# Performance work log

Measured on AMD Instinct MI355X. Metric: run time of the kernel, lower is better.

The kernel has to match this reference:

```python
import jax, jax.numpy as jnp
import numpy as np

DIM, HEADS, SEG, DIL = 1024, 16, 64, 2
B, L = 4, 4096
HEAD_DIM = DIM // HEADS
SCALE = HEAD_DIM ** -0.5


def _hilbert_map(seq_len: int) -> np.ndarray:
    # exact port of generate_hilbert_curve / hilbert_index
    size = int(np.ceil(np.sqrt(seq_len)))
    if size * size != seq_len:
        size = 2 ** int(np.ceil(np.log2(size)))

    def hidx(x, y, n):
        d = 0
        s = n // 2
        while s > 0:
            rx = 1 if (x & s) > 0 else 0
            ry = 1 if (y & s) > 0 else 0
            d += s * s * ((3 * rx) ^ ry)
            if ry == 0:
                if rx == 1:
                    x = n - 1 - x
                    y = n - 1 - y
                x, y = y, x
            s //= 2
        return d

    m = np.zeros(size * size, dtype=np.int32)
    for y in range(size):
        for x in range(size):
            m[y * size + x] = hidx(x, y, size)
    return m[:seq_len]


def setup_inputs() -> dict:
    key = jax.random.key(0)
    k1, k2, k3 = jax.random.split(key, 3)
    x = jax.random.normal(k1, (B, L, DIM), dtype=jnp.float32)
    w_qkv = jax.random.normal(k2, (DIM, 3 * DIM), dtype=jnp.float32) * 0.02
    w_proj = jax.random.normal(k3, (DIM, DIM), dtype=jnp.float32) * 0.02
    hilbert_map = jnp.asarray(_hilbert_map(L))
    return {"x": x, "w_qkv": w_qkv, "w_proj": w_proj, "hilbert_map": hilbert_map}


def reference(x, w_qkv, w_proj, hilbert_map):
    Bq, Lq, _ = x.shape
    n_seg = Lq // SEG
    # qkv projection -> [3, B, H, L, D]
    qkv = (x @ w_qkv).reshape(Bq, Lq, 3, HEADS, HEAD_DIM).transpose(2, 0, 3, 1, 4)
    q, k, v = qkv[0], qkv[1], qkv[2]
    # Hilbert reorder along sequence
    q = q[:, :, hilbert_map, :]
    k = k[:, :, hilbert_map, :]
    v = v[:, :, hilbert_map, :]
    # segmented dilated attention: [B,H,S,seg,D]
    qs = q.reshape(Bq, HEADS, n_seg, SEG, HEAD_DIM)
    ks = k.reshape(Bq, HEADS, n_seg, SEG, HEAD_DIM)[:, :, :, ::DIL, :]
    vs = v.reshape(Bq, HEADS, n_seg, SEG, HEAD_DIM)[:, :, :, ::DIL, :]
    scores = jnp.einsum('bhsqd,bhskd->bhsqk', qs, ks) * SCALE
    attn = jax.nn.softmax(scores, axis=-1)
    out = jnp.einsum('bhsqk,bhskd->bhsqd', attn, vs).reshape(Bq, HEADS, Lq, HEAD_DIM)
    # inverse Hilbert reorder
    inv = jnp.argsort(hilbert_map)
    out = out[:, :, inv, :]
    out = out.transpose(0, 2, 1, 3).reshape(Bq, Lq, DIM)
    return out @ w_proj
```

## Files before the change

### kernel.cpp

```cpp
#include <hip/hip_runtime.h>

#define L_SEQ 4096

typedef unsigned short u16;
typedef unsigned int u32;
typedef __bf16 bf16_t;
typedef bf16_t bf16x8 __attribute__((ext_vector_type(8)));
typedef float f32x4 __attribute__((ext_vector_type(4)));
typedef unsigned short u16x8 __attribute__((ext_vector_type(8)));

__device__ __forceinline__ u16 f2b(float f) {
  unsigned u = __float_as_uint(f);
  u += 0x7fffu + ((u >> 16) & 1u);
  return (u16)(u >> 16);
}
__device__ __forceinline__ float b2f(u16 b) {
  return __uint_as_float(((unsigned)b) << 16);
}

#define FENCE asm volatile("" ::: "memory")
#define BARRIER __builtin_amdgcn_s_barrier()
#define WAIT_LGKM0 asm volatile("s_waitcnt lgkmcnt(0)" ::: "memory")
#define WAIT_VM4 asm volatile("s_waitcnt vmcnt(4)" ::: "memory")
#define SB0 __builtin_amdgcn_sched_barrier(0)
#define AS1 __attribute__((address_space(1)))
#define AS3 __attribute__((address_space(3)))

__global__ __launch_bounds__(256) void k_prep(const float* __restrict__ x,
                                              u16* __restrict__ xb,
                                              const float* __restrict__ wq,
                                              u16* __restrict__ wqT,
                                              const float* __restrict__ wp,
                                              u16* __restrict__ wpT,
                                              const int* __restrict__ hmap,
                                              u16* __restrict__ xg) {
  const int bid = blockIdx.x;
  const int t = threadIdx.x;
  if (bid < 4096) {
    const int i = (bid * 256 + t) * 16;
    f32x4 v0 = *reinterpret_cast<const f32x4*>(x + i);
    f32x4 v1 = *reinterpret_cast<const f32x4*>(x + i + 4);
    f32x4 v2 = *reinterpret_cast<const f32x4*>(x + i + 8);
    f32x4 v3 = *reinterpret_cast<const f32x4*>(x + i + 12);
    u16x8 o0, o1;
#pragma unroll
    for (int j = 0; j < 4; ++j) {
      o0[j] = f2b(v0[j]); o0[4 + j] = f2b(v1[j]);
      o1[j] = f2b(v2[j]); o1[4 + j] = f2b(v3[j]);
    }
    *reinterpret_cast<u16x8*>(xb + i) = o0;
    *reinterpret_cast<u16x8*>(xb + i + 8) = o1;
    return;
  }
  if (bid >= 8192) {
    const int g = bid - 8192;
    const int gi = g * 8 + (t >> 5);
    const int lane32 = t & 31;
    const int b = gi >> 11, i = gi & 2047;
    const int s = i >> 5, j = i & 31;
    const int token = hmap[s * 64 + 2 * j];
    const float* src = x + ((size_t)(b * 4096 + token)) * 1024 + lane32 * 32;
    u16* dst = xg + (size_t)gi * 1024 + lane32 * 32;
#pragma unroll
    for (int c = 0; c < 4; ++c) {
      f32x4 v0 = *(const f32x4*)(src + c * 8);
      f32x4 v1 = *(const f32x4*)(src + c * 8 + 4);
      u16x8 o;
#pragma unroll
      for (int q = 0; q < 4; ++q) { o[q] = f2b(v0[q]); o[4 + q] = f2b(v1[q]); }
      *(u16x8*)(dst + c * 8) = o;
    }
    return;
  }
  const float* in; u16* out; int R, C, bx, by;
  if (bid < 7168) {
    const int b2 = bid - 4096;
    in = wq; out = wqT; R = 1024; C = 3072;
    bx = (b2 % 96) * 32; by = (b2 / 96) * 32;
  } else {
    const int b2 = bid - 7168;
    in = wp; out = wpT; R = 1024; C = 1024;
    bx = (b2 % 32) * 32; by = (b2 / 32) * 32;
  }
  __shared__ float tile[32][33];
  const int tx = t & 31, ty = t >> 5;
#pragma unroll
  for (int i = 0; i < 32; i += 8)
    tile[ty + i][tx] = in[(size_t)(by + ty + i) * C + (bx + tx)];
  __syncthreads();
#pragma unroll
  for (int i = 0; i < 32; i += 8)
    out[(size_t)(bx + ty + i) * R + (by + tx)] = f2b(tile[tx][ty + i]);
}

template <bool OUT_BF16>
__device__ __forceinline__ void gemm_body(char* lds, const u16* __restrict__ A,
                                          const u16* __restrict__ Bt,
                                          void* __restrict__ Cv,
                                          int N, int K, int ntiles, int gx, int bid) {
  const int tid = threadIdx.x;
  const int wid = tid >> 6, lane = tid & 63;
  const int wm = wid >> 2, wn = wid & 3;
  const int lr = lane & 15, lq = lane >> 4;
  const int xr = (lr & 7) << 4;
  const int koff0 = (lq * 16) ^ xr;
  const int koff1 = (64 | (lq * 16)) ^ xr;

  const int cpx = 32 * ntiles;
  auto tilecoord = [&](int ff, int& mm, int& nn) {
    int swz = (ff & 7) * cpx + (ff >> 3);
    mm = (swz / gx) * 256; nn = (swz % gx) * 256;
  };

  const int rowT = tid >> 3;
  const int colT = (((tid * 16) & 127) ^ ((rowT & 7) << 4)) >> 1;
  const size_t r64K = (size_t)64 * K;
  const size_t r128K = (size_t)128 * K;

  int m0, n0;
  tilecoord(bid, m0, n0);
  const u16* pAc = A + (size_t)(m0 + rowT) * K + colT;
  const u16* pBc = Bt + (size_t)(n0 + rowT) * K + colT;

  f32x4 acc[8][4];
  bf16x8 a[4][2];
  bf16x8 bb[2][2][2];

  auto STG = [&](const u16* bp, int region, size_t hoff, int k0) {
    const u16* s0 = bp + hoff + k0;
    __builtin_amdgcn_global_load_lds((const AS1 void*)s0,
                                     (AS3 void*)(lds + region + wid * 1024), 16, 0, 0);
    __builtin_amdgcn_global_load_lds((const AS1 void*)(s0 + r64K),
                                     (AS3 void*)(lds + region + 8192 + wid * 1024), 16, 0, 0);
  };
  auto rdA = [&](int dbuf, int mh) {
#pragma unroll
    for (int mi = 0; mi < 4; ++mi) {
      const int base = dbuf * 65536 + wm * 16384 + (mh * 64 + mi * 16 + lr) * 128;
      a[mi][0] = *(const bf16x8*)(lds + base + koff0);
      a[mi][1] = *(const bf16x8*)(lds + base + koff1);
    }
  };
  auto rdB = [&](int dbuf, int nh, int bset) {
#pragma unroll
    for (int ni = 0; ni < 2; ++ni) {
      const int base = dbuf * 65536 + 32768 + (wn >> 1) * 16384 +
                       ((wn & 1) * 64 + nh * 32 + ni * 16 + lr) * 128;
      bb[bset][ni][0] = *(const bf16x8*)(lds + base + koff0);
      bb[bset][ni][1] = *(const bf16x8*)(lds + base + koff1);
    }
  };
  auto mfma16 = [&](int mh, int nh, int bset) {
    __builtin_amdgcn_s_setprio(1);
#pragma unroll
    for (int kk = 0; kk < 2; ++kk)
#pragma unroll
      for (int ni = 0; ni < 2; ++ni)
#pragma unroll
        for (int mi = 0; mi < 4; ++mi)
          acc[mh * 4 + mi][nh * 2 + ni] = __builtin_amdgcn_mfma_f32_16x16x32_bf16(
              a[mi][kk], bb[bset][ni][kk], acc[mh * 4 + mi][nh * 2 + ni], 0, 0, 0);
    __builtin_amdgcn_s_setprio(0);
  };

  STG(pAc, 0,             0,     0);
  STG(pBc, 32768,         0,     0);
  STG(pBc, 49152,         r128K, 0);
  STG(pAc, 16384,         r128K, 0);
  STG(pBc, 65536 + 32768, 0,     64);
  STG(pBc, 65536 + 49152, r128K, 64);
  WAIT_VM4; FENCE; BARRIER;

  const int NT = K >> 6;
  const int NI = NT >> 1;

  for (int tt = 0; tt < ntiles; ++tt) {
    const bool hasn = (tt + 1 < ntiles);
    int m0n = m0, n0n = n0;
    if (hasn) tilecoord(bid + (tt + 1) * 256, m0n, n0n);
    const u16* pAn = hasn ? (A + (size_t)(m0n + rowT) * K + colT) : pAc;
    const u16* pBn = hasn ? (Bt + (size_t)(n0n + rowT) * K + colT) : pBc;

    {
      f32x4 z = {0.f, 0.f, 0.f, 0.f};
#pragma unroll
      for (int i = 0; i < 8; ++i)
#pragma unroll
        for (int j = 0; j < 4; ++j) acc[i][j] = z;
    }

    for (int it = 0; it < NI; ++it) {
      const int kP1 = (2 * it + 1) * 64;
      const bool last = (it == NI - 1);
      const int kA = last ? 0 : (2 * it + 2) * 64;
      const int kB = last ? 64 : (2 * it + 3) * 64;
      const u16* sA = last ? pAn : pAc;
      const u16* sB = last ? pBn : pBc;

      rdA(0, 0); rdB(0, 0, 0);
      STG(pAc, 65536, 0, kP1);
      FENCE; BARRIER; WAIT_LGKM0; SB0;
      mfma16(0, 0, 0);
      FENCE; BARRIER;
      rdB(0, 1, 1);
      STG(pAc, 65536 + 16384, r128K, kP1);
      FENCE; BARRIER; WAIT_LGKM0; SB0;
      mfma16(0, 1, 1);
      FENCE; BARRIER;
      rdA(0, 1);
      STG(sB, 32768, 0, kA);
      STG(sB, 49152, r128K, kA);
      FENCE; BARRIER; WAIT_LGKM0; SB0;
      mfma16(1, 1, 1);
      mfma16(1, 0, 0);
      WAIT_VM4; FENCE; BARRIER;
      rdA(1, 0); rdB(1, 0, 0);
      STG(sA, 0, 0, kA);
      FENCE; BARRIER; WAIT_LGKM0; SB0;
      mfma16(0, 0, 0);
      FENCE; BARRIER;
      rdB(1, 1, 1);
      STG(sA, 16384, r128K, kA);
      FENCE; BARRIER; WAIT_LGKM0; SB0;
      mfma16(0, 1, 1);
      FENCE; BARRIER;
      rdA(1, 1);
      STG(sB, 65536 + 32768, 0, kB);
      STG(sB, 65536 + 49152, r128K, kB);
      FENCE; BARRIER; WAIT_LGKM0; SB0;
      mfma16(1, 1, 1);
      mfma16(1, 0, 0);
      WAIT_VM4; FENCE; BARRIER;
    }

#pragma unroll
    for (int mi = 0; mi < 8; ++mi)
#pragma unroll
      for (int ni = 0; ni < 4; ++ni) {
        const int r0 = m0 + wm * 128 + (mi >> 2) * 64 + (mi & 3) * 16 + lq * 4;
        const int c = n0 + wn * 64 + (ni >> 1) * 32 + (ni & 1) * 16 + lr;
#pragma unroll
        for (int r = 0; r < 4; ++r) {
          const float v = acc[mi][ni][r];
          if (OUT_BF16)
            ((u16*)Cv)[(size_t)(r0 + r) * N + c] = f2b(v);
          else
            ((float*)Cv)[(size_t)(r0 + r) * N + c] = v;
        }
      }

    m0 = m0n; n0 = n0n; pAc = pAn; pBc = pBn;
  }
}

__global__ __launch_bounds__(512, 2) void k_gemm_qkv(const u16* __restrict__ xb,
                                                     const u16* __restrict__ xg,
                                                     const u16* __restrict__ wT,
                                                     u16* __restrict__ qb,
                                                     u16* __restrict__ kvb) {
  __shared__ __align__(16) char lds[131072];
  const bool kv = (blockIdx.x >= 256);
  gemm_body<true>(lds,
                  kv ? xg : xb,
                  kv ? (wT + 1024 * 1024) : wT,
                  kv ? (void*)kvb : (void*)qb,
                  kv ? 2048 : 1024, 1024, 1, kv ? 8 : 4,
                  blockIdx.x & 255);
}

__global__ __launch_bounds__(512, 2) void k_gemm_proj(const u16* __restrict__ A,
                                                      const u16* __restrict__ Bt,
                                                      float* __restrict__ C) {
  __shared__ __align__(16) char lds[131072];
  gemm_body<false>(lds, A, Bt, C, 1024, 1024, 1, 4, blockIdx.x);
}

__global__ __launch_bounds__(256) void k_attn2(const u16* __restrict__ qb,
                                               const u16* __restrict__ kvb,
                                               const int* __restrict__ hmap,
                                               u16* __restrict__ att) {
  __shared__ u16 VT[64 * 40];
  __shared__ u16 Pl[4][16 * 40];

  const int blk = blockIdx.x;
  const int b = blk >> 10, h = (blk >> 6) & 15, s = blk & 63;
  const int t = threadIdx.x, w = t >> 6, lane = t & 63;
  const int lr = lane & 15, lq = lane >> 4;
  const int* hm = hmap + s * 64;
  const size_t bb4 = (size_t)b * L_SEQ;
  const size_t kvrow0 = (size_t)(b * 2048 + s * 32);

  {
    const int kj = t >> 3, d0 = (t & 7) * 8;
    const u16* p = kvb + (kvrow0 + kj) * 2048 + 1024 + h * 64 + d0;
    u16x8 v = *(const u16x8*)p;
#pragma unroll
    for (int j = 0; j < 8; ++j) {
      const int d = d0 + j;
      const int chunk = (kj >> 3) ^ ((d >> 3) & 3);
      VT[d * 40 + chunk * 8 + (kj & 7)] = v[j];
    }
  }

  const u16* qp = qb + (bb4 + hm[16 * w + lr]) * 1024 + h * 64 + lq * 8;
  bf16x8 aq0 = *(const bf16x8*)(qp);
  bf16x8 aq1 = *(const bf16x8*)(qp + 32);
  bf16x8 bk[2][2];
#pragma unroll
  for (int nk = 0; nk < 2; ++nk) {
    const u16* kp = kvb + (kvrow0 + nk * 16 + lr) * 2048 + h * 64 + lq * 8;
    bk[nk][0] = *(const bf16x8*)(kp);
    bk[nk][1] = *(const bf16x8*)(kp + 32);
  }

  f32x4 z4 = {0.f, 0.f, 0.f, 0.f};
  f32x4 s0 = __builtin_amdgcn_mfma_f32_16x16x32_bf16(aq0, bk[0][0], z4, 0, 0, 0);
  s0 = __builtin_amdgcn_mfma_f32_16x16x32_bf16(aq1, bk[0][1], s0, 0, 0, 0);
  f32x4 s1 = __builtin_amdgcn_mfma_f32_16x16x32_bf16(aq0, bk[1][0], z4, 0, 0, 0);
  s1 = __builtin_amdgcn_mfma_f32_16x16x32_bf16(aq1, bk[1][1], s1, 0, 0, 0);

  float inv[4];
  u16* Pw = Pl[w];
#pragma unroll
  for (int r = 0; r < 4; ++r) {
    float a0 = s0[r] * 0.125f, a1 = s1[r] * 0.125f;
    float m = fmaxf(a0, a1);
    m = fmaxf(m, __shfl_xor(m, 1));
    m = fmaxf(m, __shfl_xor(m, 2));
    m = fmaxf(m, __shfl_xor(m, 4));
    m = fmaxf(m, __shfl_xor(m, 8));
    float e0 = __expf(a0 - m), e1 = __expf(a1 - m);
    float sum = e0 + e1;
    sum += __shfl_xor(sum, 1);
    sum += __shfl_xor(sum, 2);
    sum += __shfl_xor(sum, 4);
    sum += __shfl_xor(sum, 8);
    inv[r] = 1.f / sum;
    Pw[(lq * 4 + r) * 40 + lr] = f2b(e0);
    Pw[(lq * 4 + r) * 40 + 16 + lr] = f2b(e1);
  }

  __syncthreads();

  bf16x8 ap = *(const bf16x8*)(Pw + lr * 40 + lq * 8);
  f32x4 o[4];
#pragma unroll
  for (int nd = 0; nd < 4; ++nd) {
    const int row = nd * 16 + lr;
    const int chunk = lq ^ ((row >> 3) & 3);
    bf16x8 bv = *(const bf16x8*)(VT + row * 40 + chunk * 8);
    o[nd] = __builtin_amdgcn_mfma_f32_16x16x32_bf16(ap, bv, z4, 0, 0, 0);
  }

#pragma unroll
  for (int r = 0; r < 4; ++r) {
    u16* dst = att + (bb4 + hm[16 * w + lq * 4 + r]) * 1024 + h * 64 + lr;
#pragma unroll
    for (int nd = 0; nd < 4; ++nd)
      dst[nd * 16] = f2b(o[nd][r] * inv[r]);
  }
}

extern "C" void kernel_launch(void* const* d_in, const int* in_sizes, int n_in,
                              void* d_out, int out_size, void* d_ws, size_t ws_size,
                              hipStream_t stream) {
  const float* x = (const float*)d_in[0];
  const float* w_qkv = (const float*)d_in[1];
  const float* w_proj = (const float*)d_in[2];
  const int* hmap = (const int*)d_in[3];
  float* out = (float*)d_out;

  char* ws = (char*)d_ws;
  u16* qb    = (u16*)(ws);
  u16* kvb   = (u16*)(ws + 33554432ull);
  u16* xb    = (u16*)(ws + 67108864ull);
  u16* xg    = (u16*)(ws + 100663296ull);
  u16* wqkvT = (u16*)(ws + 117440512ull);
  u16* wpT   = (u16*)(ws + 123731968ull);
  u16* att = xb;

  k_prep<<<9216, 256, 0, stream>>>(x, xb, w_qkv, wqkvT, w_proj, wpT, hmap, xg);
  k_gemm_qkv<<<512, 512, 0, stream>>>(xb, xg, wqkvT, qb, kvb);
  k_attn2<<<4096, 256, 0, stream>>>(qb, kvb, hmap, att);
  k_gemm_proj<<<256, 512, 0, stream>>>(att, wpT, out);
}
```

Measured before the change: 166.5 us.

## Fuse Hilbert gather of K/V rows into QKV GEMM A-loads, drop xg buffer

Removes the prep-kernel pass that gathered and converted Hilbert-selected x rows into a separate xg buffer. The KV half of the QKV GEMM now computes per-row source pointers through hmap and loads scattered rows of xb directly into LDS. The multi-tile loop in gemm_body is also removed and each block handles exactly one tile. This saves a global read and write of about 16 MB plus 1024 prep blocks, at the cost of non-contiguous A-row loads in the GEMM.

```diff
diff --git a/kernel.cpp b/kernel.cpp
--- a/kernel.cpp
+++ b/kernel.cpp
@@ -31,9 +31,7 @@
                                               const float* __restrict__ wq,
                                               u16* __restrict__ wqT,
                                               const float* __restrict__ wp,
-                                              u16* __restrict__ wpT,
-                                              const int* __restrict__ hmap,
-                                              u16* __restrict__ xg) {
+                                              u16* __restrict__ wpT) {
   const int bid = blockIdx.x;
   const int t = threadIdx.x;
   if (bid < 4096) {
@@ -52,26 +50,6 @@
     *reinterpret_cast<u16x8*>(xb + i + 8) = o1;
     return;
   }
-  if (bid >= 8192) {
-    const int g = bid - 8192;
-    const int gi = g * 8 + (t >> 5);
-    const int lane32 = t & 31;
-    const int b = gi >> 11, i = gi & 2047;
-    const int s = i >> 5, j = i & 31;
-    const int token = hmap[s * 64 + 2 * j];
-    const float* src = x + ((size_t)(b * 4096 + token)) * 1024 + lane32 * 32;
-    u16* dst = xg + (size_t)gi * 1024 + lane32 * 32;
-#pragma unroll
-    for (int c = 0; c < 4; ++c) {
-      f32x4 v0 = *(const f32x4*)(src + c * 8);
-      f32x4 v1 = *(const f32x4*)(src + c * 8 + 4);
-      u16x8 o;
-#pragma unroll
-      for (int q = 0; q < 4; ++q) { o[q] = f2b(v0[q]); o[4 + q] = f2b(v1[q]); }
-      *(u16x8*)(dst + c * 8) = o;
-    }
-    return;
-  }
   const float* in; u16* out; int R, C, bx, by;
   if (bid < 7168) {
     const int b2 = bid - 4096;
@@ -93,11 +71,12 @@
     out[(size_t)(bx + ty + i) * R + (by + tx)] = f2b(tile[tx][ty + i]);
 }
 
-template <bool OUT_BF16>
+template <bool OUT_BF16, bool AMAP>
 __device__ __forceinline__ void gemm_body(char* lds, const u16* __restrict__ A,
                                           const u16* __restrict__ Bt,
+                                          const int* __restrict__ hmap,
                                           void* __restrict__ Cv,
-                                          int N, int K, int ntiles, int gx, int bid) {
+                                          int N, int K, int gx, int bid) {
   const int tid = threadIdx.x;
   const int wid = tid >> 6, lane = tid & 63;
   const int wm = wid >> 2, wn = wid & 3;
@@ -106,32 +85,46 @@
   const int koff0 = (lq * 16) ^ xr;
   const int koff1 = (64 | (lq * 16)) ^ xr;
 
-  const int cpx = 32 * ntiles;
-  auto tilecoord = [&](int ff, int& mm, int& nn) {
-    int swz = (ff & 7) * cpx + (ff >> 3);
-    mm = (swz / gx) * 256; nn = (swz % gx) * 256;
-  };
+  const int swz = (bid & 7) * 32 + (bid >> 3);
+  const int m0 = (swz / gx) * 256, n0 = (swz % gx) * 256;
 
   const int rowT = tid >> 3;
   const int colT = (((tid * 16) & 127) ^ ((rowT & 7) << 4)) >> 1;
   const size_t r64K = (size_t)64 * K;
   const size_t r128K = (size_t)128 * K;
 
-  int m0, n0;
-  tilecoord(bid, m0, n0);
-  const u16* pAc = A + (size_t)(m0 + rowT) * K + colT;
+  const u16 *pA0, *pA1, *pA2, *pA3;
+  if constexpr (AMAP) {
+    auto maprow = [&](int gi) -> const u16* {
+      const int token = hmap[((gi & 2047) >> 5) * 64 + 2 * (gi & 31)];
+      return A + ((size_t)((gi >> 11) * 4096 + token)) * (size_t)K + colT;
+    };
+    pA0 = maprow(m0 + rowT);
+    pA1 = maprow(m0 + 64 + rowT);
+    pA2 = maprow(m0 + 128 + rowT);
+    pA3 = maprow(m0 + 192 + rowT);
+  } else {
+    pA0 = A + (size_t)(m0 + rowT) * K + colT;
+    pA1 = pA0 + r64K; pA2 = pA0 + r128K; pA3 = pA2 + r64K;
+  }
   const u16* pBc = Bt + (size_t)(n0 + rowT) * K + colT;
 
   f32x4 acc[8][4];
   bf16x8 a[4][2];
   bf16x8 bb[2][2][2];
 
-  auto STG = [&](const u16* bp, int region, size_t hoff, int k0) {
-    const u16* s0 = bp + hoff + k0;
+  auto LDS1 = [&](const u16* s0, int region) {
     __builtin_amdgcn_global_load_lds((const AS1 void*)s0,
                                      (AS3 void*)(lds + region + wid * 1024), 16, 0, 0);
-    __builtin_amdgcn_global_load_lds((const AS1 void*)(s0 + r64K),
-                                     (AS3 void*)(lds + region + 8192 + wid * 1024), 16, 0, 0);
+  };
+  auto STG_A0 = [&](int region, int k0) {
+    LDS1(pA0 + k0, region); LDS1(pA1 + k0, region + 8192);
+  };
+  auto STG_A1 = [&](int region, int k0) {
+    LDS1(pA2 + k0, region); LDS1(pA3 + k0, region + 8192);
+  };
+  auto STG_B = [&](int region, size_t hoff, int k0) {
+    LDS1(pBc + hoff + k0, region); LDS1(pBc + hoff + r64K + k0, region + 8192);
   };
   auto rdA = [&](int dbuf, int mh) {
 #pragma unroll
@@ -163,116 +156,101 @@
     __builtin_amdgcn_s_setprio(0);
   };
 
-  STG(pAc, 0,             0,     0);
-  STG(pBc, 32768,         0,     0);
-  STG(pBc, 49152,         r128K, 0);
-  STG(pAc, 16384,         r128K, 0);
-  STG(pBc, 65536 + 32768, 0,     64);
-  STG(pBc, 65536 + 49152, r128K, 64);
+  {
+    f32x4 z = {0.f, 0.f, 0.f, 0.f};
+#pragma unroll
+    for (int i = 0; i < 8; ++i)
+#pragma unroll
+      for (int j = 0; j < 4; ++j) acc[i][j] = z;
+  }
+
+  STG_A0(0, 0);
+  STG_B(32768, 0, 0);
+  STG_B(49152, r128K, 0);
+  STG_A1(16384, 0);
+  STG_B(65536 + 32768, 0, 64);
+  STG_B(65536 + 49152, r128K, 64);
   WAIT_VM4; FENCE; BARRIER;
 
-  const int NT = K >> 6;
-  const int NI = NT >> 1;
-
-  for (int tt = 0; tt < ntiles; ++tt) {
-    const bool hasn = (tt + 1 < ntiles);
-    int m0n = m0, n0n = n0;
-    if (hasn) tilecoord(bid + (tt + 1) * 256, m0n, n0n);
-    const u16* pAn = hasn ? (A + (size_t)(m0n + rowT) * K + colT) : pAc;
-    const u16* pBn = hasn ? (Bt + (size_t)(n0n + rowT) * K + colT) : pBc;
-
-    {
-      f32x4 z = {0.f, 0.f, 0.f, 0.f};
-#pragma unroll
-      for (int i = 0; i < 8; ++i)
-#pragma unroll
-        for (int j = 0; j < 4; ++j) acc[i][j] = z;
-    }
-
-    for (int it = 0; it < NI; ++it) {
-      const int kP1 = (2 * it + 1) * 64;
-      const bool last = (it == NI - 1);
-      const int kA = last ? 0 : (2 * it + 2) * 64;
-      const int kB = last ? 64 : (2 * it + 3) * 64;
-      const u16* sA = last ? pAn : pAc;
-      const u16* sB = last ? pBn : pBc;
-
-      rdA(0, 0); rdB(0, 0, 0);
-      STG(pAc, 65536, 0, kP1);
-      FENCE; BARRIER; WAIT_LGKM0; SB0;
-      mfma16(0, 0, 0);
-      FENCE; BARRIER;
-      rdB(0, 1, 1);
-      STG(pAc, 65536 + 16384, r128K, kP1);
-      FENCE; BARRIER; WAIT_LGKM0; SB0;
-      mfma16(0, 1, 1);
-      FENCE; BARRIER;
-      rdA(0, 1);
-      STG(sB, 32768, 0, kA);
-      STG(sB, 49152, r128K, kA);
-      FENCE; BARRIER; WAIT_LGKM0; SB0;
-      mfma16(1, 1, 1);
-      mfma16(1, 0, 0);
-      WAIT_VM4; FENCE; BARRIER;
-      rdA(1, 0); rdB(1, 0, 0);
-      STG(sA, 0, 0, kA);
-      FENCE; BARRIER; WAIT_LGKM0; SB0;
-      mfma16(0, 0, 0);
-      FENCE; BARRIER;
-      rdB(1, 1, 1);
-      STG(sA, 16384, r128K, kA);
-      FENCE; BARRIER; WAIT_LGKM0; SB0;
-      mfma16(0, 1, 1);
-      FENCE; BARRIER;
-      rdA(1, 1);
-      STG(sB, 65536 + 32768, 0, kB);
-      STG(sB, 65536 + 49152, r128K, kB);
-      FENCE; BARRIER; WAIT_LGKM0; SB0;
-      mfma16(1, 1, 1);
-      mfma16(1, 0, 0);
-      WAIT_VM4; FENCE; BARRIER;
-    }
-
-#pragma unroll
-    for (int mi = 0; mi < 8; ++mi)
-#pragma unroll
-      for (int ni = 0; ni < 4; ++ni) {
-        const int r0 = m0 + wm * 128 + (mi >> 2) * 64 + (mi & 3) * 16 + lq * 4;
-        const int c = n0 + wn * 64 + (ni >> 1) * 32 + (ni & 1) * 16 + lr;
-#pragma unroll
-        for (int r = 0; r < 4; ++r) {
-          const float v = acc[mi][ni][r];
-          if (OUT_BF16)
-            ((u16*)Cv)[(size_t)(r0 + r) * N + c] = f2b(v);
-          else
-            ((float*)Cv)[(size_t)(r0 + r) * N + c] = v;
-        }
+  const int NI = K >> 7;
+
+  for (int it = 0; it < NI; ++it) {
+    const int kP1 = (2 * it + 1) * 64;
+    const bool last = (it == NI - 1);
+    const int kA = last ? 0 : (2 * it + 2) * 64;
+    const int kB = last ? 64 : (2 * it + 3) * 64;
+
+    rdA(0, 0); rdB(0, 0, 0);
+    STG_A0(65536, kP1);
+    FENCE; BARRIER; WAIT_LGKM0; SB0;
+    mfma16(0, 0, 0);
+    FENCE; BARRIER;
+    rdB(0, 1, 1);
+    STG_A1(65536 + 16384, kP1);
+    FENCE; BARRIER; WAIT_LGKM0; SB0;
+    mfma16(0, 1, 1);
+    FENCE; BARRIER;
+    rdA(0, 1);
+    STG_B(32768, 0, kA);
+    STG_B(49152, r128K, kA);
+    FENCE; BARRIER; WAIT_LGKM0; SB0;
+    mfma16(1, 1, 1);
+    mfma16(1, 0, 0);
+    WAIT_VM4; FENCE; BARRIER;
+    rdA(1, 0); rdB(1, 0, 0);
+    STG_A0(0, kA);
+    FENCE; BARRIER; WAIT_LGKM0; SB0;
+    mfma16(0, 0, 0);
+    FENCE; BARRIER;
+    rdB(1, 1, 1);
+    STG_A1(16384, kA);
+    FENCE; BARRIER; WAIT_LGKM0; SB0;
+    mfma16(0, 1, 1);
+    FENCE; BARRIER;
+    rdA(1, 1);
+    STG_B(65536 + 32768, 0, kB);
+    STG_B(65536 + 49152, r128K, kB);
+    FENCE; BARRIER; WAIT_LGKM0; SB0;
+    mfma16(1, 1, 1);
+    mfma16(1, 0, 0);
+    WAIT_VM4; FENCE; BARRIER;
+  }
+
+#pragma unroll
+  for (int mi = 0; mi < 8; ++mi)
+#pragma unroll
+    for (int ni = 0; ni < 4; ++ni) {
+      const int r0 = m0 + wm * 128 + (mi >> 2) * 64 + (mi & 3) * 16 + lq * 4;
+      const int c = n0 + wn * 64 + (ni >> 1) * 32 + (ni & 1) * 16 + lr;
+#pragma unroll
+      for (int r = 0; r < 4; ++r) {
+        const float v = acc[mi][ni][r];
+        if (OUT_BF16)
+          ((u16*)Cv)[(size_t)(r0 + r) * N + c] = f2b(v);
+        else
+          ((float*)Cv)[(size_t)(r0 + r) * N + c] = v;
       }
-
-    m0 = m0n; n0 = n0n; pAc = pAn; pBc = pBn;
-  }
+    }
 }
 
 __global__ __launch_bounds__(512, 2) void k_gemm_qkv(const u16* __restrict__ xb,
-                                                     const u16* __restrict__ xg,
                                                      const u16* __restrict__ wT,
+                                                     const int* __restrict__ hmap,
                                                      u16* __restrict__ qb,
                                                      u16* __restrict__ kvb) {
   __shared__ __align__(16) char lds[131072];
-  const bool kv = (blockIdx.x >= 256);
-  gemm_body<true>(lds,
-                  kv ? xg : xb,
-                  kv ? (wT + 1024 * 1024) : wT,
-                  kv ? (void*)kvb : (void*)qb,
-                  kv ? 2048 : 1024, 1024, 1, kv ? 8 : 4,
-                  blockIdx.x & 255);
+  if (blockIdx.x >= 256)
+    gemm_body<true, true>(lds, xb, wT + 1024 * 1024, hmap, kvb, 2048, 1024, 8,
+                          blockIdx.x & 255);
+  else
+    gemm_body<true, false>(lds, xb, wT, nullptr, qb, 1024, 1024, 4, blockIdx.x);
 }
 
 __global__ __launch_bounds__(512, 2) void k_gemm_proj(const u16* __restrict__ A,
                                                       const u16* __restrict__ Bt,
                                                       float* __restrict__ C) {
   __shared__ __align__(16) char lds[131072];
-  gemm_body<false>(lds, A, Bt, C, 1024, 1024, 1, 4, blockIdx.x);
+  gemm_body<false, false>(lds, A, Bt, nullptr, C, 1024, 1024, 4, blockIdx.x);
 }
 
 __global__ __launch_bounds__(256) void k_attn2(const u16* __restrict__ qb,
@@ -374,13 +352,12 @@
   u16* qb    = (u16*)(ws);
   u16* kvb   = (u16*)(ws + 33554432ull);
   u16* xb    = (u16*)(ws + 67108864ull);
-  u16* xg    = (u16*)(ws + 100663296ull);
-  u16* wqkvT = (u16*)(ws + 117440512ull);
-  u16* wpT   = (u16*)(ws + 123731968ull);
+  u16* wqkvT = (u16*)(ws + 100663296ull);
+  u16* wpT   = (u16*)(ws + 106954752ull);
   u16* att = xb;
 
-  k_prep<<<9216, 256, 0, stream>>>(x, xb, w_qkv, wqkvT, w_proj, wpT, hmap, xg);
-  k_gemm_qkv<<<512, 512, 0, stream>>>(xb, xg, wqkvT, qb, kvb);
+  k_prep<<<8192, 256, 0, stream>>>(x, xb, w_qkv, wqkvT, w_proj, wpT);
+  k_gemm_qkv<<<512, 512, 0, stream>>>(xb, wqkvT, hmap, qb, kvb);
   k_attn2<<<4096, 256, 0, stream>>>(qb, kvb, hmap, att);
   k_gemm_proj<<<256, 512, 0, stream>>>(att, wpT, out);
 }
```

Result: faster. 154.6 us, median of 2 (-7.1%).
